# Performance work log

Measured on AMD Instinct MI355X. Metric: run time of the kernel, lower is better.

## Reference

```python
import jax, jax.numpy as jnp
import numpy as np

K = 512  # num codes
COMMITMENT_COST = 0.25

def setup_inputs() -> dict:
    key = jax.random.key(0)
    k1, k2 = jax.random.split(key)
    z = jax.random.normal(k1, (64, 64, 64, 64), dtype=jnp.float32)   # (B, C=D, H, W)
    emb = jax.random.normal(k2, (K, 64), dtype=jnp.float32)          # codebook (K, D)
    return {"z": z, "emb": emb}

def reference(z, emb):
    B, C, H, W = z.shape
    z_nhwc = jnp.transpose(z, (0, 2, 3, 1))            # (B, H, W, C)
    zf = z_nhwc.reshape(-1, C)                          # (BHW, C)
    # squared-distance matrix: ||z||^2 + ||e||^2 - 2 z.e  -> (BHW, K)
    dist = (jnp.sum(zf * zf, axis=1, keepdims=True)
            + jnp.sum(emb * emb, axis=1)
            - 2.0 * jnp.einsum('bd,kd->bk', zf, emb))
    idx = jnp.argmin(dist, axis=1)                      # (BHW,)
    enc = jax.nn.one_hot(idx, K, dtype=z.dtype)         # (BHW, K)
    avg_use = jnp.mean(enc, axis=0)
    perplexity = jnp.exp(-jnp.sum(avg_use * jnp.log(avg_use + 1e-10)))
    z_q = emb[idx].reshape(B, H, W, C)                  # gathered codes
    sg = jax.lax.stop_gradient
    loss = (COMMITMENT_COST * jnp.mean((sg(z_q) - z_nhwc) ** 2)
            + jnp.mean((z_q - sg(z_nhwc)) ** 2))
    z_q_ste = z_nhwc + sg(z_q - z_nhwc)                 # straight-through
    z_q_out = jnp.transpose(z_q_ste, (0, 3, 1, 2))      # (B, C, H, W)
    idx_out = idx.reshape(B, H, W)
    return z_q_out, loss, idx_out, perplexity
```

## Files before the change

kernel.cpp:

```cpp
#include <hip/hip_runtime.h>

#define ZQ_OFF    0
#define LOSS_OFF  16777216
#define IDX_OFF   16777217
#define PERP_OFF  17039361

#define NPOINTS   262144
#define NELEM     16777216


__global__ void prep_kernel(const float* __restrict__ emb,
                            float* __restrict__ embnorm,
                            int* __restrict__ hist,
                            double* __restrict__ lossacc) {
    int k = threadIdx.x;
    hist[k] = 0;
    const float* e = emb + (k << 6);
    float s = 0.f;
    #pragma unroll
    for (int d = 0; d < 64; ++d) s += e[d] * e[d];
    embnorm[k] = s;
    if (k == 0) *lossacc = 0.0;
}

__global__ __launch_bounds__(256, 4) void vq_kernel(const float* __restrict__ z,
                                                 const float* __restrict__ emb,
                                                 const float* __restrict__ embnorm,
                                                 float* __restrict__ out,
                                                 int* __restrict__ hist,
                                                 double* __restrict__ lossacc) {
    const int bid = blockIdx.x;
    const int b  = bid >> 4;
    const int h  = ((bid & 15) << 2) + (threadIdx.x >> 6);
    const int w  = threadIdx.x & 63;

    const float* zp = z + ((size_t)b << 18) + ((size_t)h << 6) + w;
    float zv[64];
    float z2 = 0.f;
    #pragma unroll
    for (int d = 0; d < 64; ++d) {
        float v = zp[(size_t)d << 12];
        zv[d] = v;
        z2 += v * v;
    }

    float best = 3.4e38f;
    int   bidx = 0;
    for (int k0 = 0; k0 < 512; k0 += 4) {
        const float* e0 = emb + ((size_t)k0 << 6);
        float a0 = 0.f, a1 = 0.f, a2 = 0.f, a3 = 0.f;
        #pragma unroll
        for (int d = 0; d < 64; ++d) {
            float v = zv[d];
            a0 += v * e0[d];
            a1 += v * e0[d + 64];
            a2 += v * e0[d + 128];
            a3 += v * e0[d + 192];
        }
        float d0 = z2 + embnorm[k0    ] - 2.f * a0;
        float d1 = z2 + embnorm[k0 + 1] - 2.f * a1;
        float d2 = z2 + embnorm[k0 + 2] - 2.f * a2;
        float d3 = z2 + embnorm[k0 + 3] - 2.f * a3;
        if (d0 < best) { best = d0; bidx = k0;     }
        if (d1 < best) { best = d1; bidx = k0 + 1; }
        if (d2 < best) { best = d2; bidx = k0 + 2; }
        if (d3 < best) { best = d3; bidx = k0 + 3; }
    }

    const size_t pidx = ((size_t)b << 12) + ((size_t)h << 6) + w;
    __builtin_nontemporal_store((float)bidx, &out[IDX_OFF + pidx]);
    atomicAdd(&hist[bidx], 1);

    const float* eb = emb + ((size_t)bidx << 6);
    float* zqout = out + ((size_t)b << 18) + ((size_t)h << 6) + w;
    float lsum = 0.f;
    #pragma unroll
    for (int d = 0; d < 64; ++d) {
        float e    = eb[d];
        float diff = e - zv[d];
        lsum += diff * diff;
        __builtin_nontemporal_store(zv[d] + diff, &zqout[(size_t)d << 12]);
    }

    #pragma unroll
    for (int off = 32; off; off >>= 1) lsum += __shfl_down(lsum, off, 64);
    __shared__ float wsum[4];
    if ((threadIdx.x & 63) == 0) wsum[threadIdx.x >> 6] = lsum;
    __syncthreads();
    if (threadIdx.x == 0) {
        atomicAdd(lossacc, (double)(wsum[0] + wsum[1] + wsum[2] + wsum[3]));
    }
}

__global__ void fin_kernel(const int* __restrict__ hist,
                           const double* __restrict__ lossacc,
                           float* __restrict__ out) {
    int k = threadIdx.x;
    float avg = (float)hist[k] * (1.0f / 262144.0f);
    float t = avg * logf(avg + 1e-10f);
    #pragma unroll
    for (int off = 32; off; off >>= 1) t += __shfl_down(t, off, 64);
    __shared__ float s[8];
    if ((k & 63) == 0) s[k >> 6] = t;
    __syncthreads();
    if (k == 0) {
        float S = 0.f;
        #pragma unroll
        for (int i = 0; i < 8; ++i) S += s[i];
        out[PERP_OFF] = expf(-S);
        out[LOSS_OFF] = (float)(1.25 * (*lossacc) / (double)NELEM);
    }
}

extern "C" void kernel_launch(void* const* d_in, const int* in_sizes, int n_in,
                              void* d_out, int out_size, void* d_ws, size_t ws_size,
                              hipStream_t stream) {
    const float* z   = (const float*)d_in[0];
    const float* emb = (const float*)d_in[1];
    float* out = (float*)d_out;

    float*  embnorm = (float*)d_ws;
    int*    hist    = (int*)((char*)d_ws + 2048);
    double* lossacc = (double*)((char*)d_ws + 4096);

    prep_kernel<<<1, 512, 0, stream>>>(emb, embnorm, hist, lossacc);
    vq_kernel<<<1024, 256, 0, stream>>>(z, emb, embnorm, out, hist, lossacc);
    fin_kernel<<<1, 512, 0, stream>>>(hist, lossacc, out);
}
```

Before: 527.9 us.

## Stage codebook tiles in LDS and use 1024-thread blocks

New measurement: 653.4 us. +23.8%, slower.

```diff
diff --git a/kernel.cpp b/kernel.cpp
--- a/kernel.cpp
+++ b/kernel.cpp
@@ -7,6 +7,7 @@
 
 #define NPOINTS   262144
 #define NELEM     16777216
+#define KTILE     256
 
 
 __global__ void prep_kernel(const float* __restrict__ emb,
@@ -23,16 +24,18 @@
     if (k == 0) *lossacc = 0.0;
 }
 
-__global__ __launch_bounds__(256, 4) void vq_kernel(const float* __restrict__ z,
+__global__ __launch_bounds__(1024, 4) void vq_kernel(const float* __restrict__ z,
                                                  const float* __restrict__ emb,
                                                  const float* __restrict__ embnorm,
                                                  float* __restrict__ out,
                                                  int* __restrict__ hist,
                                                  double* __restrict__ lossacc) {
+    __shared__ __align__(16) float elds[KTILE * 64];
+    const int tid = threadIdx.x;
     const int bid = blockIdx.x;
-    const int b  = bid >> 4;
-    const int h  = ((bid & 15) << 2) + (threadIdx.x >> 6);
-    const int w  = threadIdx.x & 63;
+    const int b  = bid >> 2;
+    const int h  = ((bid & 3) << 4) + (tid >> 6);
+    const int w  = tid & 63;
 
     const float* zp = z + ((size_t)b << 18) + ((size_t)h << 6) + w;
     float zv[64];
@@ -46,25 +49,40 @@
 
     float best = 3.4e38f;
     int   bidx = 0;
-    for (int k0 = 0; k0 < 512; k0 += 4) {
-        const float* e0 = emb + ((size_t)k0 << 6);
-        float a0 = 0.f, a1 = 0.f, a2 = 0.f, a3 = 0.f;
+
+    for (int t = 0; t < 512; t += KTILE) {
+        __syncthreads();
+        const float4* esrc = (const float4*)(emb + ((size_t)t << 6));
+        float4*       edst = (float4*)elds;
         #pragma unroll
-        for (int d = 0; d < 64; ++d) {
-            float v = zv[d];
-            a0 += v * e0[d];
-            a1 += v * e0[d + 64];
-            a2 += v * e0[d + 128];
-            a3 += v * e0[d + 192];
+        for (int i = 0; i < 4; ++i)
+            edst[tid + (i << 10)] = esrc[tid + (i << 10)];
+        __syncthreads();
+
+        for (int k0 = 0; k0 < KTILE; k0 += 4) {
+            const float* e0 = elds + (k0 << 6);
+            float a0 = 0.f, a1 = 0.f, a2 = 0.f, a3 = 0.f;
+            #pragma unroll
+            for (int dc = 0; dc < 64; dc += 4) {
+                float4 e0v = *(const float4*)(e0 + dc);
+                float4 e1v = *(const float4*)(e0 + 64 + dc);
+                float4 e2v = *(const float4*)(e0 + 128 + dc);
+                float4 e3v = *(const float4*)(e0 + 192 + dc);
+                a0 += zv[dc] * e0v.x; a0 += zv[dc+1] * e0v.y; a0 += zv[dc+2] * e0v.z; a0 += zv[dc+3] * e0v.w;
+                a1 += zv[dc] * e1v.x; a1 += zv[dc+1] * e1v.y; a1 += zv[dc+2] * e1v.z; a1 += zv[dc+3] * e1v.w;
+                a2 += zv[dc] * e2v.x; a2 += zv[dc+1] * e2v.y; a2 += zv[dc+2] * e2v.z; a2 += zv[dc+3] * e2v.w;
+                a3 += zv[dc] * e3v.x; a3 += zv[dc+1] * e3v.y; a3 += zv[dc+2] * e3v.z; a3 += zv[dc+3] * e3v.w;
+            }
+            int kk = t + k0;
+            float d0 = z2 + embnorm[kk    ] - 2.f * a0;
+            float d1 = z2 + embnorm[kk + 1] - 2.f * a1;
+            float d2 = z2 + embnorm[kk + 2] - 2.f * a2;
+            float d3 = z2 + embnorm[kk + 3] - 2.f * a3;
+            if (d0 < best) { best = d0; bidx = kk;     }
+            if (d1 < best) { best = d1; bidx = kk + 1; }
+            if (d2 < best) { best = d2; bidx = kk + 2; }
+            if (d3 < best) { best = d3; bidx = kk + 3; }
         }
-        float d0 = z2 + embnorm[k0    ] - 2.f * a0;
-        float d1 = z2 + embnorm[k0 + 1] - 2.f * a1;
-        float d2 = z2 + embnorm[k0 + 2] - 2.f * a2;
-        float d3 = z2 + embnorm[k0 + 3] - 2.f * a3;
-        if (d0 < best) { best = d0; bidx = k0;     }
-        if (d1 < best) { best = d1; bidx = k0 + 1; }
-        if (d2 < best) { best = d2; bidx = k0 + 2; }
-        if (d3 < best) { best = d3; bidx = k0 + 3; }
     }
 
     const size_t pidx = ((size_t)b << 12) + ((size_t)h << 6) + w;
@@ -84,11 +102,15 @@
 
     #pragma unroll
     for (int off = 32; off; off >>= 1) lsum += __shfl_down(lsum, off, 64);
-    __shared__ float wsum[4];
-    if ((threadIdx.x & 63) == 0) wsum[threadIdx.x >> 6] = lsum;
     __syncthreads();
-    if (threadIdx.x == 0) {
-        atomicAdd(lossacc, (double)(wsum[0] + wsum[1] + wsum[2] + wsum[3]));
+    float* wsum = elds;
+    if ((tid & 63) == 0) wsum[tid >> 6] = lsum;
+    __syncthreads();
+    if (tid == 0) {
+        float s = 0.f;
+        #pragma unroll
+        for (int i = 0; i < 16; ++i) s += wsum[i];
+        atomicAdd(lossacc, (double)s);
     }
 }
 
@@ -124,6 +146,6 @@
     double* lossacc = (double*)((char*)d_ws + 4096);
 
     prep_kernel<<<1, 512, 0, stream>>>(emb, embnorm, hist, lossacc);
-    vq_kernel<<<1024, 256, 0, stream>>>(z, emb, embnorm, out, hist, lossacc);
+    vq_kernel<<<256, 1024, 0, stream>>>(z, emb, embnorm, out, hist, lossacc);
     fin_kernel<<<1, 512, 0, stream>>>(hist, lossacc, out);
 }
```
